# Kernel optimization log

Measured on AMD Instinct MI355X. Metric: run time of the kernel, lower is better.

## Reference

```python
import jax, jax.numpy as jnp
import numpy as np

N_EMBD = 1024
N_HEAD = 16
B, T = 4, 2048

def setup_inputs() -> dict:
    key = jax.random.key(0)
    ks = jax.random.split(key, 5)
    s = 0.02
    return {
        "x": jax.random.normal(ks[0], (B, T, N_EMBD), dtype=jnp.float32),
        "w_attn": jax.random.normal(ks[1], (N_EMBD, 3 * N_EMBD), dtype=jnp.float32) * s,
        "b_attn": jnp.zeros((3 * N_EMBD,), dtype=jnp.float32),
        "w_proj": jax.random.normal(ks[2], (N_EMBD, N_EMBD), dtype=jnp.float32) * s,
        "b_proj": jnp.zeros((N_EMBD,), dtype=jnp.float32),
    }

def reference(x, w_attn, b_attn, w_proj, b_proj):
    Bx, Tx, C = x.shape
    hd = C // N_HEAD
    qkv = x @ w_attn + b_attn  # [B,T,3C]
    q, k, v = jnp.split(qkv, 3, axis=-1)
    # [B,H,T,hd]
    q = q.reshape(Bx, Tx, N_HEAD, hd).transpose(0, 2, 1, 3)
    k = k.reshape(Bx, Tx, N_HEAD, hd).transpose(0, 2, 1, 3)
    v = v.reshape(Bx, Tx, N_HEAD, hd).transpose(0, 2, 1, 3)
    scale = 1.0 / np.sqrt(hd).astype(np.float32)
    wei = jnp.einsum('bhqd,bhkd->bhqk', q, k) * scale
    causal = jnp.tril(jnp.ones((Tx, Tx), dtype=bool))
    wei = jnp.where(causal[None, None], wei, jnp.float32(-jnp.inf))
    wei = jax.nn.softmax(wei, axis=-1)
    out = jnp.einsum('bhqk,bhkd->bhqd', wei, v)
    out = out.transpose(0, 2, 1, 3).reshape(Bx, Tx, C)
    return out @ w_proj + b_proj
```

## Files before the change

kernel.cpp:

```cpp
#include <hip/hip_runtime.h>
#include <hip/hip_bf16.h>
#include <math.h>

#define BB 4
#define TT 2048
#define CC 1024
#define HH 16
#define HD 64
#define C3 3072
#define MM (BB * TT)

typedef __attribute__((ext_vector_type(8))) short bf16x8;
typedef __attribute__((ext_vector_type(4))) float f32x4;
typedef __attribute__((ext_vector_type(4))) short s16x4;

__device__ inline short f32_to_bf16_bits(float f) {
    unsigned u = __float_as_uint(f);
    u += 0x7fffu + ((u >> 16) & 1u);
    return (short)(u >> 16);
}

__device__ inline void async_copy16(const void* g, void* l) {
    __builtin_amdgcn_global_load_lds((const __attribute__((address_space(1))) void*)g,
                                     (__attribute__((address_space(3))) void*)l, 16, 0, 0);
}

__global__ __launch_bounds__(256) void cast_x(const float* __restrict__ in,
                                              short* __restrict__ out) {
    int i = (blockIdx.x * 256 + threadIdx.x) * 8;
    float4 a = *(const float4*)(in + i);
    float4 b = *(const float4*)(in + i + 4);
    bf16x8 o;
    o[0] = f32_to_bf16_bits(a.x); o[1] = f32_to_bf16_bits(a.y);
    o[2] = f32_to_bf16_bits(a.z); o[3] = f32_to_bf16_bits(a.w);
    o[4] = f32_to_bf16_bits(b.x); o[5] = f32_to_bf16_bits(b.y);
    o[6] = f32_to_bf16_bits(b.z); o[7] = f32_to_bf16_bits(b.w);
    *(bf16x8*)(out + i) = o;
}

__global__ __launch_bounds__(256) void tcast(const float* __restrict__ w,
                                             short* __restrict__ wt,
                                             int K, int N) {
    __shared__ short tile[64][68];
    const int n0 = blockIdx.x * 64, k0 = blockIdx.y * 64;
    const int tid = threadIdx.x;
#pragma unroll
    for (int it = 0; it < 4; ++it) {
        int idx = it * 1024 + tid * 4;
        int r = idx >> 6, c = idx & 63;
        float4 v = *(const float4*)&w[(size_t)(k0 + r) * N + n0 + c];
        tile[r][c + 0] = f32_to_bf16_bits(v.x);
        tile[r][c + 1] = f32_to_bf16_bits(v.y);
        tile[r][c + 2] = f32_to_bf16_bits(v.z);
        tile[r][c + 3] = f32_to_bf16_bits(v.w);
    }
    __syncthreads();
#pragma unroll
    for (int it = 0; it < 4; ++it) {
        int idx = it * 256 + tid;
        int rr = idx >> 4, kc = (idx & 15) * 4;
        s16x4 o = { tile[kc + 0][rr], tile[kc + 1][rr], tile[kc + 2][rr], tile[kc + 3][rr] };
        *(s16x4*)&wt[(size_t)(n0 + rr) * K + k0 + kc] = o;
    }
}

template <bool QKV>
__global__ __launch_bounds__(256) void gemm128(const short* __restrict__ A,
                                               const short* __restrict__ Bt,
                                               const float* __restrict__ bias,
                                               short* __restrict__ qb,
                                               short* __restrict__ kb,
                                               short* __restrict__ vt,
                                               float* __restrict__ out,
                                               int N, int Kdim) {
    __shared__ __align__(16) short As[128 * 64];
    __shared__ __align__(16) short Bs[128 * 64];
    const int tid = threadIdx.x;
    const int wave = tid >> 6, lane = tid & 63;
    const int quad = lane >> 4, l16 = lane & 15;
    const int wm = wave >> 1, wn = wave & 1;
    const int m0 = blockIdx.y * 128, n0 = blockIdx.x * 128;

    f32x4 acc[4][4] = {};

    for (int k0 = 0; k0 < Kdim; k0 += 64) {
#pragma unroll
        for (int c2 = 0; c2 < 4; ++c2) {
            int g = (wave * 4 + c2) * 64 + lane;
            int row = g >> 3;
            int seg = (g & 7) ^ (row & 7);
            async_copy16(A + (size_t)(m0 + row) * Kdim + k0 + seg * 8, As + g * 8);
            async_copy16(Bt + (size_t)(n0 + row) * Kdim + k0 + seg * 8, Bs + g * 8);
        }
        __syncthreads();
#pragma unroll
        for (int ks = 0; ks < 2; ++ks) {
            bf16x8 af[4], bfv[4];
#pragma unroll
            for (int i = 0; i < 4; ++i) {
                int row = wm * 64 + i * 16 + l16;
                int u = (ks * 4 + quad) ^ (row & 7);
                af[i] = *(const bf16x8*)&As[row * 64 + u * 8];
            }
#pragma unroll
            for (int j = 0; j < 4; ++j) {
                int row = wn * 64 + j * 16 + l16;
                int u = (ks * 4 + quad) ^ (row & 7);
                bfv[j] = *(const bf16x8*)&Bs[row * 64 + u * 8];
            }
#pragma unroll
            for (int i = 0; i < 4; ++i)
#pragma unroll
                for (int j = 0; j < 4; ++j)
                    acc[i][j] = __builtin_amdgcn_mfma_f32_16x16x32_bf16(af[i], bfv[j], acc[i][j], 0, 0, 0);
        }
        __syncthreads();
    }

#pragma unroll
    for (int i = 0; i < 4; ++i)
#pragma unroll
        for (int j = 0; j < 4; ++j) {
            int n = n0 + wn * 64 + j * 16 + l16;
            float bv = bias[n];
            if (QKV) {
                int which = n >> 10, cc = n & 1023;
                int h = cc >> 6, d = cc & 63;
                if (which == 2) {
                    int m_base = m0 + wm * 64 + i * 16 + quad * 4;
                    int bb = m_base >> 11, t0 = m_base & 2047;
                    unsigned p0 = ((unsigned)(unsigned short)f32_to_bf16_bits(acc[i][j][0] + bv)) |
                                  ((unsigned)(unsigned short)f32_to_bf16_bits(acc[i][j][1] + bv) << 16);
                    unsigned p1 = ((unsigned)(unsigned short)f32_to_bf16_bits(acc[i][j][2] + bv)) |
                                  ((unsigned)(unsigned short)f32_to_bf16_bits(acc[i][j][3] + bv) << 16);
                    uint2 pk = {p0, p1};
                    *(uint2*)(vt + (((size_t)bb * HH + h) * HD + d) * TT + t0) = pk;
                } else {
#pragma unroll
                    for (int r = 0; r < 4; ++r) {
                        int m = m0 + wm * 64 + i * 16 + quad * 4 + r;
                        int bb = m >> 11, t = m & 2047;
                        short val = f32_to_bf16_bits((acc[i][j][r] + bv) * (which == 0 ? 0.125f : 1.0f));
                        size_t off = (((size_t)bb * HH + h) * TT + t) * HD + d;
                        if (which == 0) qb[off] = val;
                        else kb[off] = val;
                    }
                }
            } else {
#pragma unroll
                for (int r = 0; r < 4; ++r) {
                    int m = m0 + wm * 64 + i * 16 + quad * 4 + r;
                    out[(size_t)m * N + n] = acc[i][j][r] + bv;
                }
            }
        }
}

__global__ __launch_bounds__(512, 4) void flash_attn(const short* __restrict__ qb,
                                                     const short* __restrict__ kb,
                                                     const short* __restrict__ vt,
                                                     short* __restrict__ ab) {
    __shared__ __align__(16) short Ksh[2][4096];
    __shared__ __align__(16) short Vsh[2][4096];
    __shared__ __align__(16) short plds[8][16][72];

    const int tid = threadIdx.x;
    const int wave = tid >> 6;
    const int lane = tid & 63;
    const int quad = lane >> 4;
    const int l16 = lane & 15;

    const int bh = blockIdx.y;
    const int i = blockIdx.x;
    const int njt = 32 - 2 * i;
    const int q_lo = i * 128 + wave * 16;
    const int q_hi = (15 - i) * 128 + wave * 16;

    const short* qball = qb + (size_t)bh * TT * HD;
    const short* kball = kb + (size_t)bh * TT * HD;
    const short* vtall = vt + (size_t)bh * HD * TT;

    const int sidx = wave * 64 + lane;
    const int srow = sidx >> 3;
    const int sseg = (sidx & 7) ^ (srow & 7);
    const short* kgsrc = kball + (size_t)srow * HD + sseg * 8;
    const short* vgsrc = vtall + (size_t)srow * TT + sseg * 8;

    bf16x8 qfh[2], qfl[2];
#pragma unroll
    for (int h = 0; h < 2; ++h) {
        qfh[h] = *(const bf16x8*)(qball + (size_t)(q_hi + l16) * HD + h * 32 + quad * 8);
        qfl[h] = *(const bf16x8*)(qball + (size_t)(q_lo + l16) * HD + h * 32 + quad * 8);
    }

    f32x4 o_hi[4] = {}, o_lo[4] = {};
    float ls_hi[4] = {0.f, 0.f, 0.f, 0.f}, ls_lo[4] = {0.f, 0.f, 0.f, 0.f};

    async_copy16(kgsrc, &Ksh[0][wave * 512]);
    async_copy16(vgsrc, &Vsh[0][wave * 512]);
    __syncthreads();

    for (int jt = 0; jt < njt; ++jt) {
        const int buf = jt & 1;
        if (jt + 1 < njt) {
            async_copy16(kgsrc + (size_t)(jt + 1) * 64 * HD, &Ksh[buf ^ 1][wave * 512]);
            async_copy16(vgsrc + (jt + 1) * 64, &Vsh[buf ^ 1][wave * 512]);
        }
        const int j0 = jt * 64;

        if (j0 <= q_hi + 15) {
            f32x4 s[4];
#pragma unroll
            for (int cb = 0; cb < 4; ++cb) {
                int row = cb * 16 + l16;
                bf16x8 k0 = *(const bf16x8*)&Ksh[buf][(row * 8 + (quad ^ (row & 7))) * 8];
                bf16x8 k1 = *(const bf16x8*)&Ksh[buf][(row * 8 + ((4 + quad) ^ (row & 7))) * 8];
                f32x4 a = {};
                a = __builtin_amdgcn_mfma_f32_16x16x32_bf16(qfh[0], k0, a, 0, 0, 0);
                a = __builtin_amdgcn_mfma_f32_16x16x32_bf16(qfh[1], k1, a, 0, 0, 0);
                s[cb] = a;
            }
            if (j0 + 64 > q_hi) {
#pragma unroll
                for (int cb = 0; cb < 4; ++cb) {
                    int j = j0 + cb * 16 + l16;
#pragma unroll
                    for (int r = 0; r < 4; ++r)
                        if (j > q_hi + quad * 4 + r) s[cb][r] = -1e30f;
                }
            }
#pragma unroll
            for (int cb = 0; cb < 4; ++cb)
#pragma unroll
                for (int r = 0; r < 4; ++r) {
                    float p = __expf(s[cb][r]);
                    ls_hi[r] += p;
                    plds[wave][quad * 4 + r][cb * 16 + l16] = f32_to_bf16_bits(p);
                }
            bf16x8 pa0 = *(const bf16x8*)&plds[wave][l16][quad * 8];
            bf16x8 pa1 = *(const bf16x8*)&plds[wave][l16][32 + quad * 8];
#pragma unroll
            for (int db = 0; db < 4; ++db) {
                int row = db * 16 + l16;
                bf16x8 v0 = *(const bf16x8*)&Vsh[buf][(row * 8 + (quad ^ (row & 7))) * 8];
                bf16x8 v1 = *(const bf16x8*)&Vsh[buf][(row * 8 + ((4 + quad) ^ (row & 7))) * 8];
                o_hi[db] = __builtin_amdgcn_mfma_f32_16x16x32_bf16(pa0, v0, o_hi[db], 0, 0, 0);
                o_hi[db] = __builtin_amdgcn_mfma_f32_16x16x32_bf16(pa1, v1, o_hi[db], 0, 0, 0);
            }
        }

        if (j0 <= q_lo + 15) {
            f32x4 s[4];
#pragma unroll
            for (int cb = 0; cb < 4; ++cb) {
                int row = cb * 16 + l16;
                bf16x8 k0 = *(const bf16x8*)&Ksh[buf][(row * 8 + (quad ^ (row & 7))) * 8];
                bf16x8 k1 = *(const bf16x8*)&Ksh[buf][(row * 8 + ((4 + quad) ^ (row & 7))) * 8];
                f32x4 a = {};
                a = __builtin_amdgcn_mfma_f32_16x16x32_bf16(qfl[0], k0, a, 0, 0, 0);
                a = __builtin_amdgcn_mfma_f32_16x16x32_bf16(qfl[1], k1, a, 0, 0, 0);
                s[cb] = a;
            }
            if (j0 + 64 > q_lo) {
#pragma unroll
                for (int cb = 0; cb < 4; ++cb) {
                    int j = j0 + cb * 16 + l16;
#pragma unroll
                    for (int r = 0; r < 4; ++r)
                        if (j > q_lo + quad * 4 + r) s[cb][r] = -1e30f;
                }
            }
#pragma unroll
            for (int cb = 0; cb < 4; ++cb)
#pragma unroll
                for (int r = 0; r < 4; ++r) {
                    float p = __expf(s[cb][r]);
                    ls_lo[r] += p;
                    plds[wave][quad * 4 + r][cb * 16 + l16] = f32_to_bf16_bits(p);
                }
            bf16x8 pa0 = *(const bf16x8*)&plds[wave][l16][quad * 8];
            bf16x8 pa1 = *(const bf16x8*)&plds[wave][l16][32 + quad * 8];
#pragma unroll
            for (int db = 0; db < 4; ++db) {
                int row = db * 16 + l16;
                bf16x8 v0 = *(const bf16x8*)&Vsh[buf][(row * 8 + (quad ^ (row & 7))) * 8];
                bf16x8 v1 = *(const bf16x8*)&Vsh[buf][(row * 8 + ((4 + quad) ^ (row & 7))) * 8];
                o_lo[db] = __builtin_amdgcn_mfma_f32_16x16x32_bf16(pa0, v0, o_lo[db], 0, 0, 0);
                o_lo[db] = __builtin_amdgcn_mfma_f32_16x16x32_bf16(pa1, v1, o_lo[db], 0, 0, 0);
            }
        }
        __syncthreads();
    }

    const int b = bh >> 4, hd0 = (bh & 15) * HD;
    float inv_h[4], inv_l[4];
#pragma unroll
    for (int r = 0; r < 4; ++r) {
        float th = ls_hi[r], tl = ls_lo[r];
#pragma unroll
        for (int off = 1; off < 16; off <<= 1) {
            th += __shfl_xor(th, off, 64);
            tl += __shfl_xor(tl, off, 64);
        }
        inv_h[r] = 1.0f / th;
        inv_l[r] = 1.0f / tl;
    }
#pragma unroll
    for (int r = 0; r < 4; ++r) {
        int qh = q_hi + quad * 4 + r;
        int ql = q_lo + quad * 4 + r;
#pragma unroll
        for (int db = 0; db < 4; ++db) {
            ab[((size_t)(b * TT + qh)) * CC + hd0 + db * 16 + l16] =
                f32_to_bf16_bits(o_hi[db][r] * inv_h[r]);
            ab[((size_t)(b * TT + ql)) * CC + hd0 + db * 16 + l16] =
                f32_to_bf16_bits(o_lo[db][r] * inv_l[r]);
        }
    }
}

extern "C" void kernel_launch(void* const* d_in, const int* in_sizes, int n_in,
                              void* d_out, int out_size, void* d_ws, size_t ws_size,
                              hipStream_t stream) {
    const float* x      = (const float*)d_in[0];
    const float* w_attn = (const float*)d_in[1];
    const float* b_attn = (const float*)d_in[2];
    const float* w_proj = (const float*)d_in[3];
    const float* b_proj = (const float*)d_in[4];
    float* out = (float*)d_out;

    const size_t per = (size_t)BB * HH * TT * HD;
    short* xb      = (short*)d_ws;
    short* wt_attn = xb + per;
    short* wt_proj = wt_attn + (size_t)C3 * CC;
    short* qb      = wt_proj + (size_t)CC * CC;
    short* kb      = qb + per;
    short* vt      = kb + per;
    short* ab      = vt + per;

    cast_x<<<dim3(MM * CC / (256 * 8)), 256, 0, stream>>>(x, xb);
    tcast<<<dim3(C3 / 64, CC / 64), 256, 0, stream>>>(w_attn, wt_attn, CC, C3);
    tcast<<<dim3(CC / 64, CC / 64), 256, 0, stream>>>(w_proj, wt_proj, CC, CC);

    gemm128<true><<<dim3(C3 / 128, MM / 128), 256, 0, stream>>>(
        xb, wt_attn, b_attn, qb, kb, vt, nullptr, C3, CC);

    flash_attn<<<dim3(8, BB * HH), 512, 0, stream>>>(qb, kb, vt, ab);

    gemm128<false><<<dim3(CC / 128, MM / 128), 256, 0, stream>>>(
        ab, wt_proj, b_proj, nullptr, nullptr, nullptr, out, CC, CC);
}
```

Before: 173.3 us.

## Fold log2e into Q scale, use raw exp2, packed bf16 convert, finer waitcnt sync

Q is now prescaled by 0.125*log2(e), so the raw v_exp_f32 (exp2) instruction replaces __expf. P is staged through LDS as fp32 and packed to bf16 with v_cvt_pk_bf16_f32 instead of the manual rounding bit trick. The blanket __syncthreads is replaced by an explicit vmcnt wait plus s_barrier, letting the prefetch of the next tile stay in flight while the current one is consumed. MFMA sections are wrapped in s_setprio. The fp32 P buffer doubles LDS use per wave, which may affect occupancy, and the hand-counted vmcnt values must match the number of outstanding loads.

```diff
diff --git a/kernel.cpp b/kernel.cpp
--- a/kernel.cpp
+++ b/kernel.cpp
@@ -140,7 +140,8 @@
                     for (int r = 0; r < 4; ++r) {
                         int m = m0 + wm * 64 + i * 16 + quad * 4 + r;
                         int bb = m >> 11, t = m & 2047;
-                        short val = f32_to_bf16_bits((acc[i][j][r] + bv) * (which == 0 ? 0.125f : 1.0f));
+                        short val = f32_to_bf16_bits((acc[i][j][r] + bv) *
+                                                     (which == 0 ? 0.18033688011112042f : 1.0f));
                         size_t off = (((size_t)bb * HH + h) * TT + t) * HD + d;
                         if (which == 0) qb[off] = val;
                         else kb[off] = val;
@@ -162,7 +163,7 @@
                                                      short* __restrict__ ab) {
     __shared__ __align__(16) short Ksh[2][4096];
     __shared__ __align__(16) short Vsh[2][4096];
-    __shared__ __align__(16) short plds[8][16][72];
+    __shared__ __align__(16) float plds[8][16][68];
 
     const int tid = threadIdx.x;
     const int wave = tid >> 6;
@@ -198,18 +199,25 @@
 
     async_copy16(kgsrc, &Ksh[0][wave * 512]);
     async_copy16(vgsrc, &Vsh[0][wave * 512]);
-    __syncthreads();
 
     for (int jt = 0; jt < njt; ++jt) {
         const int buf = jt & 1;
         if (jt + 1 < njt) {
             async_copy16(kgsrc + (size_t)(jt + 1) * 64 * HD, &Ksh[buf ^ 1][wave * 512]);
             async_copy16(vgsrc + (jt + 1) * 64, &Vsh[buf ^ 1][wave * 512]);
-        }
+            asm volatile("s_waitcnt vmcnt(2)" : : : "memory");
+        } else {
+            asm volatile("s_waitcnt vmcnt(0)" : : : "memory");
+        }
+        __builtin_amdgcn_sched_barrier(0);
+        __builtin_amdgcn_s_barrier();
+        __builtin_amdgcn_sched_barrier(0);
+
         const int j0 = jt * 64;
 
         if (j0 <= q_hi + 15) {
             f32x4 s[4];
+            __builtin_amdgcn_s_setprio(1);
 #pragma unroll
             for (int cb = 0; cb < 4; ++cb) {
                 int row = cb * 16 + l16;
@@ -220,6 +228,7 @@
                 a = __builtin_amdgcn_mfma_f32_16x16x32_bf16(qfh[1], k1, a, 0, 0, 0);
                 s[cb] = a;
             }
+            __builtin_amdgcn_s_setprio(0);
             if (j0 + 64 > q_hi) {
 #pragma unroll
                 for (int cb = 0; cb < 4; ++cb) {
@@ -233,24 +242,43 @@
             for (int cb = 0; cb < 4; ++cb)
 #pragma unroll
                 for (int r = 0; r < 4; ++r) {
-                    float p = __expf(s[cb][r]);
+                    float p;
+                    asm("v_exp_f32 %0, %1" : "=v"(p) : "v"(s[cb][r]));
                     ls_hi[r] += p;
-                    plds[wave][quad * 4 + r][cb * 16 + l16] = f32_to_bf16_bits(p);
-                }
-            bf16x8 pa0 = *(const bf16x8*)&plds[wave][l16][quad * 8];
-            bf16x8 pa1 = *(const bf16x8*)&plds[wave][l16][32 + quad * 8];
-#pragma unroll
-            for (int db = 0; db < 4; ++db) {
-                int row = db * 16 + l16;
-                bf16x8 v0 = *(const bf16x8*)&Vsh[buf][(row * 8 + (quad ^ (row & 7))) * 8];
-                bf16x8 v1 = *(const bf16x8*)&Vsh[buf][(row * 8 + ((4 + quad) ^ (row & 7))) * 8];
-                o_hi[db] = __builtin_amdgcn_mfma_f32_16x16x32_bf16(pa0, v0, o_hi[db], 0, 0, 0);
-                o_hi[db] = __builtin_amdgcn_mfma_f32_16x16x32_bf16(pa1, v1, o_hi[db], 0, 0, 0);
+                    plds[wave][quad * 4 + r][cb * 16 + l16] = p;
+                }
+            {
+                const float* prow = &plds[wave][l16][0];
+                f32x4 pr0 = *(const f32x4*)(prow + quad * 8);
+                f32x4 pr1 = *(const f32x4*)(prow + quad * 8 + 4);
+                f32x4 pr2 = *(const f32x4*)(prow + 32 + quad * 8);
+                f32x4 pr3 = *(const f32x4*)(prow + 32 + quad * 8 + 4);
+                union { unsigned u[4]; bf16x8 v; } pa0u, pa1u;
+                asm("v_cvt_pk_bf16_f32 %0, %1, %2" : "=v"(pa0u.u[0]) : "v"(pr0[0]), "v"(pr0[1]));
+                asm("v_cvt_pk_bf16_f32 %0, %1, %2" : "=v"(pa0u.u[1]) : "v"(pr0[2]), "v"(pr0[3]));
+                asm("v_cvt_pk_bf16_f32 %0, %1, %2" : "=v"(pa0u.u[2]) : "v"(pr1[0]), "v"(pr1[1]));
+                asm("v_cvt_pk_bf16_f32 %0, %1, %2" : "=v"(pa0u.u[3]) : "v"(pr1[2]), "v"(pr1[3]));
+                asm("v_cvt_pk_bf16_f32 %0, %1, %2" : "=v"(pa1u.u[0]) : "v"(pr2[0]), "v"(pr2[1]));
+                asm("v_cvt_pk_bf16_f32 %0, %1, %2" : "=v"(pa1u.u[1]) : "v"(pr2[2]), "v"(pr2[3]));
+                asm("v_cvt_pk_bf16_f32 %0, %1, %2" : "=v"(pa1u.u[2]) : "v"(pr3[0]), "v"(pr3[1]));
+                asm("v_cvt_pk_bf16_f32 %0, %1, %2" : "=v"(pa1u.u[3]) : "v"(pr3[2]), "v"(pr3[3]));
+                bf16x8 pa0 = pa0u.v, pa1 = pa1u.v;
+                __builtin_amdgcn_s_setprio(1);
+#pragma unroll
+                for (int db = 0; db < 4; ++db) {
+                    int row = db * 16 + l16;
+                    bf16x8 v0 = *(const bf16x8*)&Vsh[buf][(row * 8 + (quad ^ (row & 7))) * 8];
+                    bf16x8 v1 = *(const bf16x8*)&Vsh[buf][(row * 8 + ((4 + quad) ^ (row & 7))) * 8];
+                    o_hi[db] = __builtin_amdgcn_mfma_f32_16x16x32_bf16(pa0, v0, o_hi[db], 0, 0, 0);
+                    o_hi[db] = __builtin_amdgcn_mfma_f32_16x16x32_bf16(pa1, v1, o_hi[db], 0, 0, 0);
+                }
+                __builtin_amdgcn_s_setprio(0);
             }
         }
 
         if (j0 <= q_lo + 15) {
             f32x4 s[4];
+            __builtin_amdgcn_s_setprio(1);
 #pragma unroll
             for (int cb = 0; cb < 4; ++cb) {
                 int row = cb * 16 + l16;
@@ -261,6 +289,7 @@
                 a = __builtin_amdgcn_mfma_f32_16x16x32_bf16(qfl[1], k1, a, 0, 0, 0);
                 s[cb] = a;
             }
+            __builtin_amdgcn_s_setprio(0);
             if (j0 + 64 > q_lo) {
 #pragma unroll
                 for (int cb = 0; cb < 4; ++cb) {
@@ -274,22 +303,41 @@
             for (int cb = 0; cb < 4; ++cb)
 #pragma unroll
                 for (int r = 0; r < 4; ++r) {
-                    float p = __expf(s[cb][r]);
+                    float p;
+                    asm("v_exp_f32 %0, %1" : "=v"(p) : "v"(s[cb][r]));
                     ls_lo[r] += p;
-                    plds[wave][quad * 4 + r][cb * 16 + l16] = f32_to_bf16_bits(p);
-                }
-            bf16x8 pa0 = *(const bf16x8*)&plds[wave][l16][quad * 8];
-            bf16x8 pa1 = *(const bf16x8*)&plds[wave][l16][32 + quad * 8];
-#pragma unroll
-            for (int db = 0; db < 4; ++db) {
-                int row = db * 16 + l16;
-                bf16x8 v0 = *(const bf16x8*)&Vsh[buf][(row * 8 + (quad ^ (row & 7))) * 8];
-                bf16x8 v1 = *(const bf16x8*)&Vsh[buf][(row * 8 + ((4 + quad) ^ (row & 7))) * 8];
-                o_lo[db] = __builtin_amdgcn_mfma_f32_16x16x32_bf16(pa0, v0, o_lo[db], 0, 0, 0);
-                o_lo[db] = __builtin_amdgcn_mfma_f32_16x16x32_bf16(pa1, v1, o_lo[db], 0, 0, 0);
-            }
-        }
-        __syncthreads();
+                    plds[wave][quad * 4 + r][cb * 16 + l16] = p;
+                }
+            {
+                const float* prow = &plds[wave][l16][0];
+                f32x4 pr0 = *(const f32x4*)(prow + quad * 8);
+                f32x4 pr1 = *(const f32x4*)(prow + quad * 8 + 4);
+                f32x4 pr2 = *(const f32x4*)(prow + 32 + quad * 8);
+                f32x4 pr3 = *(const f32x4*)(prow + 32 + quad * 8 + 4);
+                union { unsigned u[4]; bf16x8 v; } pa0u, pa1u;
+                asm("v_cvt_pk_bf16_f32 %0, %1, %2" : "=v"(pa0u.u[0]) : "v"(pr0[0]), "v"(pr0[1]));
+                asm("v_cvt_pk_bf16_f32 %0, %1, %2" : "=v"(pa0u.u[1]) : "v"(pr0[2]), "v"(pr0[3]));
+                asm("v_cvt_pk_bf16_f32 %0, %1, %2" : "=v"(pa0u.u[2]) : "v"(pr1[0]), "v"(pr1[1]));
+                asm("v_cvt_pk_bf16_f32 %0, %1, %2" : "=v"(pa0u.u[3]) : "v"(pr1[2]), "v"(pr1[3]));
+                asm("v_cvt_pk_bf16_f32 %0, %1, %2" : "=v"(pa1u.u[0]) : "v"(pr2[0]), "v"(pr2[1]));
+                asm("v_cvt_pk_bf16_f32 %0, %1, %2" : "=v"(pa1u.u[1]) : "v"(pr2[2]), "v"(pr2[3]));
+                asm("v_cvt_pk_bf16_f32 %0, %1, %2" : "=v"(pa1u.u[2]) : "v"(pr3[0]), "v"(pr3[1]));
+                asm("v_cvt_pk_bf16_f32 %0, %1, %2" : "=v"(pa1u.u[3]) : "v"(pr3[2]), "v"(pr3[3]));
+                bf16x8 pa0 = pa0u.v, pa1 = pa1u.v;
+                __builtin_amdgcn_s_setprio(1);
+#pragma unroll
+                for (int db = 0; db < 4; ++db) {
+                    int row = db * 16 + l16;
+                    bf16x8 v0 = *(const bf16x8*)&Vsh[buf][(row * 8 + (quad ^ (row & 7))) * 8];
+                    bf16x8 v1 = *(const bf16x8*)&Vsh[buf][(row * 8 + ((4 + quad) ^ (row & 7))) * 8];
+                    o_lo[db] = __builtin_amdgcn_mfma_f32_16x16x32_bf16(pa0, v0, o_lo[db], 0, 0, 0);
+                    o_lo[db] = __builtin_amdgcn_mfma_f32_16x16x32_bf16(pa1, v1, o_lo[db], 0, 0, 0);
+                }
+                __builtin_amdgcn_s_setprio(0);
+            }
+        }
+        __builtin_amdgcn_sched_barrier(0);
+        __builtin_amdgcn_s_barrier();
     }
 
     const int b = bh >> 4, hd0 = (bh & 15) * HD;
```

Result: faster. 168.8 us (-2.6%).
